# Optimization experiments

Measured on AMD Instinct MI355X. Metric: run time of the kernel, lower is better.

Reference implementation:

```python
import jax, jax.numpy as jnp
import numpy as np

EMBED_DIM = 64
GAMMA = 1.0
N_X = 8192
N_Y = 8192


def _self_attention(inputs, W_q, W_k):
    # inputs: [n, d]; W_q, W_k: [d, d]
    q = inputs @ W_q
    k = inputs @ W_k
    scores = jax.nn.softmax(q @ k.T / jnp.sqrt(jnp.float32(EMBED_DIM)), axis=-1)  # [n, n]
    return scores @ inputs  # [n, d]


def setup_inputs() -> dict:
    key = jax.random.key(0)
    k1, k2, k3, k4 = jax.random.split(key, 4)
    return {
        "rotation_params": jax.random.normal(k1, (EMBED_DIM, EMBED_DIM), dtype=jnp.float32),
        "entangle_params": jax.random.normal(k2, (EMBED_DIM, EMBED_DIM), dtype=jnp.float32),
        "x": jax.random.normal(k3, (N_X, EMBED_DIM), dtype=jnp.float32),
        "y": jax.random.normal(k4, (N_Y, EMBED_DIM), dtype=jnp.float32),
    }


def reference(rotation_params, entangle_params, x, y):
    x_att = _self_attention(x, rotation_params, entangle_params)  # [n_x, d]
    y_att = _self_attention(y, rotation_params, entangle_params)  # [n_y, d]
    # Pairwise squared distances, vectorizing the original per-pair loop.
    diff = x_att[:, None, :] - y_att[None, :, :]  # [n_x, n_y, d]
    sq = jnp.sum(diff * diff, axis=-1)  # [n_x, n_y]
    return jnp.exp(-GAMMA * sq)
```

## Files before the change

### kernel.cpp

```cpp
#include <hip/hip_runtime.h>
#include <math.h>

#define N 8192
#define D 64
#define LOG2E 1.4426950408889634f

typedef _Float16 half_t;
typedef _Float16 f16x8 __attribute__((ext_vector_type(8)));
typedef _Float16 f16x4 __attribute__((ext_vector_type(4)));
typedef float f32x4 __attribute__((ext_vector_type(4)));

#define MFMA32(a, b, c) __builtin_amdgcn_mfma_f32_16x16x32_f16((a), (b), (c), 0, 0, 0)

#define SPLIT(v, H, L) { half_t _h = (half_t)(v); (H) = _h; (L) = (half_t)((v) - (float)_h); }


__global__ __launch_bounds__(256) void proj_kernel(
    const float* __restrict__ Wq, const float* __restrict__ Wk,
    const float* __restrict__ X, const float* __restrict__ Y,
    float* __restrict__ Qx, float* __restrict__ Qy,
    half_t* __restrict__ Kfx, half_t* __restrict__ Kfy)
{
    __shared__ float sWq[64][64];
    __shared__ float sWk[64][64];
    __shared__ float sIn[16][64];
    const int t = threadIdx.x;
#pragma unroll
    for (int p = 0; p < 16; ++p) {
        int idx = p * 256 + t;
        sWq[idx >> 6][idx & 63] = Wq[idx];
        sWk[idx >> 6][idx & 63] = Wk[idx];
    }
    const int R0 = blockIdx.x * 16;
    const float* src; float* dq; half_t* dkf; int r0;
    if (R0 < N) { src = X; dq = Qx; dkf = Kfx; r0 = R0; }
    else        { src = Y; dq = Qy; dkf = Kfy; r0 = R0 - N; }
#pragma unroll
    for (int p = 0; p < 4; ++p) {
        int idx = p * 256 + t;
        sIn[idx >> 6][idx & 63] = src[(size_t)r0 * D + idx];
    }
    __syncthreads();
    const int c = t & 63;
    const int rb = t >> 6;
    const int ksi = c >> 5, quadi = (c >> 3) & 3, j = c & 7;
#pragma unroll
    for (int rr = 0; rr < 4; ++rr) {
        int r = rr * 4 + rb;
        float aq = 0.f, ak = 0.f;
#pragma unroll
        for (int k = 0; k < 64; ++k) {
            float xv = sIn[r][k];
            aq = fmaf(xv, sWq[k][c], aq);
            ak = fmaf(xv, sWk[k][c], ak);
        }
        int rg = r0 + r;
        dq[(size_t)rg * D + c] = aq * (0.125f * LOG2E);
        int tile = rg >> 5, tau = (rg >> 4) & 1, c16l = rg & 15;
        size_t kidx = (size_t)tile * 4096 + ksi * 2048 + tau * 1024
                    + (quadi * 16 + c16l) * 8 + j;
        half_t hh = (half_t)ak;
        dkf[kidx]       = hh;
        dkf[kidx + 512] = (half_t)(ak - (float)hh);
    }
}

__global__ __launch_bounds__(256) void ztprep_kernel(
    const float* __restrict__ X, const float* __restrict__ Y,
    half_t* __restrict__ Zfx, half_t* __restrict__ Zfy)
{
    const int t = threadIdx.x;
    const int tile = blockIdx.x;
    const float* src = blockIdx.y ? Y : X;
    half_t* dst = blockIdx.y ? Zfy : Zfx;
    const int dt = t >> 6, lane = t & 63;
    const int quad = lane >> 4, c16 = lane & 15;
    f16x8 h;
#pragma unroll
    for (int j = 0; j < 8; ++j)
        h[j] = (half_t)src[(size_t)(tile * 32 + quad * 8 + j) * D + dt * 16 + c16];
    *(f16x8*)&dst[(size_t)tile * 2048 + dt * 512 + lane * 8] = h;
}

template<int KS>
__global__ __launch_bounds__(256, 2) void attn_kernel(
    const float* __restrict__ Qx, const float* __restrict__ Qy,
    const half_t* __restrict__ Kfx, const half_t* __restrict__ Kfy,
    const half_t* __restrict__ Zfx, const half_t* __restrict__ Zfy,
    float* __restrict__ Opart, float* __restrict__ mpart, float* __restrict__ lpart)
{
    const int side = blockIdx.y;
    const float*  Q  = side ? Qy  : Qx;
    const half_t* Kf = side ? Kfy : Kfx;
    const half_t* Zf = side ? Zfy : Zfx;
    const int t = threadIdx.x, w = t >> 6, lane = t & 63;
    const int c16 = lane & 15, quad = lane >> 4;
    const int q0 = blockIdx.x * 128 + w * 32;
    const int tile0 = blockIdx.z * (N / KS / 32);
    const int ITERS = (N / KS) / 32;

    __shared__ half_t Pbuf[4][32][40];
    half_t (*Phi)[40] = Pbuf[w];

    f16x8 qh[2][2], ql[2][2];
#pragma unroll
    for (int qg = 0; qg < 2; ++qg)
#pragma unroll
        for (int ks = 0; ks < 2; ++ks) {
            const float* s = &Q[(size_t)(q0 + 16 * qg + c16) * D + ks * 32 + quad * 8];
            f32x4 v0 = *(const f32x4*)s;
            f32x4 v1 = *(const f32x4*)(s + 4);
            f16x8 h, l;
#pragma unroll
            for (int i = 0; i < 4; ++i) { SPLIT(v0[i], h[i],     l[i]); }
#pragma unroll
            for (int i = 0; i < 4; ++i) { SPLIT(v1[i], h[4 + i], l[4 + i]); }
            qh[qg][ks] = h; ql[qg][ks] = l;
        }

    f32x4 ot[4][2] = {};
    f32x4 lacc[2] = {};
    float m_run[2] = {-INFINITY, -INFINITY};
    f16x8 ones;
#pragma unroll
    for (int i = 0; i < 8; ++i) ones[i] = (half_t)1.0f;

    f16x8 kAh[2][2], kAl[2][2], kBh[2][2], kBl[2][2];
    f32x4 st[2][2];

    auto loadK = [&](int tile, f16x8 (&kh)[2][2], f16x8 (&kl)[2][2]) {
        const half_t* b = Kf + (size_t)tile * 4096 + lane * 8;
#pragma unroll
        for (int ks = 0; ks < 2; ++ks)
#pragma unroll
            for (int tau = 0; tau < 2; ++tau) {
                kh[ks][tau] = *(const f16x8*)&b[ks * 2048 + tau * 1024];
                kl[ks][tau] = *(const f16x8*)&b[ks * 2048 + tau * 1024 + 512];
            }
    };
    auto doS = [&](f16x8 (&kh)[2][2], f16x8 (&kl)[2][2]) {
        const f32x4 zero = {};
#pragma unroll
        for (int qg = 0; qg < 2; ++qg)
#pragma unroll
            for (int tau = 0; tau < 2; ++tau) st[qg][tau] = zero;
#pragma unroll
        for (int ks = 0; ks < 2; ++ks)
#pragma unroll
            for (int tau = 0; tau < 2; ++tau)
#pragma unroll
                for (int qg = 0; qg < 2; ++qg) {
                    st[qg][tau] = MFMA32(kh[ks][tau], qh[qg][ks], st[qg][tau]);
                    st[qg][tau] = MFMA32(kh[ks][tau], ql[qg][ks], st[qg][tau]);
                    st[qg][tau] = MFMA32(kl[ks][tau], qh[qg][ks], st[qg][tau]);
                }
    };

    auto body = [&](int tt, f16x8 (&kh2)[2][2], f16x8 (&kl2)[2][2]) {
        const int tile = tile0 + tt;
        const half_t* zb = Zf + (size_t)tile * 2048 + lane * 8;
        f16x8 zh[4];
#pragma unroll
        for (int dt = 0; dt < 4; ++dt)
            zh[dt] = *(const f16x8*)&zb[dt * 512];
        const bool more = (tt + 1 < ITERS);
        if (more) loadK(tile + 1, kh2, kl2);
#pragma unroll
        for (int qg = 0; qg < 2; ++qg) {
            float mt = fmaxf(fmaxf(fmaxf(st[qg][0][0], st[qg][0][1]),
                                   fmaxf(st[qg][0][2], st[qg][0][3])),
                             fmaxf(fmaxf(st[qg][1][0], st[qg][1][1]),
                                   fmaxf(st[qg][1][2], st[qg][1][3])));
            mt = fmaxf(mt, __shfl_xor(mt, 16));
            mt = fmaxf(mt, __shfl_xor(mt, 32));
            float mn = fmaxf(m_run[qg], mt);
            float al = exp2f(m_run[qg] - mn);
            m_run[qg] = mn;
#pragma unroll
            for (int tau = 0; tau < 2; ++tau) {
                f16x4 h4;
#pragma unroll
                for (int r = 0; r < 4; ++r)
                    h4[r] = (half_t)exp2f(st[qg][tau][r] - mn);
                *(f16x4*)&Phi[16 * qg + c16][16 * tau + 4 * quad] = h4;
            }
            lacc[qg] *= al;
#pragma unroll
            for (int dt = 0; dt < 4; ++dt) ot[dt][qg] *= al;
        }
        f16x8 pbh[2];
#pragma unroll
        for (int qg = 0; qg < 2; ++qg)
            pbh[qg] = *(const f16x8*)&Phi[16 * qg + c16][quad * 8];
#pragma unroll
        for (int dt = 0; dt < 4; ++dt)
#pragma unroll
            for (int qg = 0; qg < 2; ++qg)
                ot[dt][qg] = MFMA32(zh[dt], pbh[qg], ot[dt][qg]);
#pragma unroll
        for (int qg = 0; qg < 2; ++qg)
            lacc[qg] = MFMA32(ones, pbh[qg], lacc[qg]);
        if (more) doS(kh2, kl2);
    };

    loadK(tile0, kAh, kAl);
    doS(kAh, kAl);
#pragma unroll 1
    for (int tt = 0; tt < ITERS; tt += 2) {
        body(tt,     kBh, kBl);
        body(tt + 1, kAh, kAl);
    }

    const size_t obase = (size_t)(side * KS + blockIdx.z) * N;
#pragma unroll
    for (int qg = 0; qg < 2; ++qg) {
        int q = q0 + 16 * qg + c16;
#pragma unroll
        for (int dt = 0; dt < 4; ++dt)
            *(f32x4*)&Opart[(obase + q) * D + 16 * dt + 4 * quad] = ot[dt][qg];
        if (quad == 0) {
            mpart[obase + q] = m_run[qg];
            lpart[obase + q] = lacc[qg][0];
        }
    }
}

template<int KS>
__global__ __launch_bounds__(256) void combine_kernel(
    const float* __restrict__ Opart, const float* __restrict__ mpart,
    const float* __restrict__ lpart,
    half_t* __restrict__ Xf, half_t* __restrict__ Yf,
    float* __restrict__ n2x, float* __restrict__ n2y)
{
    const int side = blockIdx.y;
    const int q = blockIdx.x * 16 + (threadIdx.x >> 4);
    const int d4 = (threadIdx.x & 15) * 4;
    float m[KS], l[KS];
#pragma unroll
    for (int s = 0; s < KS; ++s) {
        size_t b = (size_t)(side * KS + s) * N + q;
        m[s] = mpart[b]; l[s] = lpart[b];
    }
    float M = -INFINITY;
#pragma unroll
    for (int s = 0; s < KS; ++s) M = fmaxf(M, m[s]);
    float L = 0.f;
    f32x4 o = {0.f, 0.f, 0.f, 0.f};
#pragma unroll
    for (int s = 0; s < KS; ++s) {
        float sc = exp2f(m[s] - M);
        L += l[s] * sc;
        f32x4 p = *(const f32x4*)&Opart[((size_t)(side * KS + s) * N + q) * D + d4];
        o += p * sc;
    }
    float inv = 1.f / L;
    o *= inv;
    float sq = o[0] * o[0] + o[1] * o[1] + o[2] * o[2] + o[3] * o[3];
#pragma unroll
    for (int off = 1; off < 16; off <<= 1) sq += __shfl_xor(sq, off);
    half_t* dst = side ? Yf : Xf;
    float*  n2  = side ? n2y : n2x;
    if ((threadIdx.x & 15) == 0) n2[q] = sq * LOG2E;
    const float oscale = side ? 1.0f : 2.0f * LOG2E;
    f16x4 h4, l4;
#pragma unroll
    for (int i = 0; i < 4; ++i) { float v = o[i] * oscale; SPLIT(v, h4[i], l4[i]); }
    const int tile16 = q >> 4, c16l = q & 15;
    const int ksi = d4 >> 5, quadi = (d4 >> 3) & 3, j0 = d4 & 7;
    size_t idx = (size_t)tile16 * 2048 + ksi * 1024 + (quadi * 16 + c16l) * 8 + j0;
    *(f16x4*)&dst[idx]       = h4;
    *(f16x4*)&dst[idx + 512] = l4;
}

__global__ __launch_bounds__(256, 3) void rbf_kernel(
    const half_t* __restrict__ Xf, const half_t* __restrict__ Yf,
    const float* __restrict__ n2x, const float* __restrict__ n2y,
    float* __restrict__ out)
{
    const int t = threadIdx.x, w = t >> 6, lane = t & 63;
    const int c16 = lane & 15, quad = lane >> 4;
    const int X0 = blockIdx.y * 128 + (w >> 1) * 64;
    const int Y0 = blockIdx.x * 128 + (w & 1) * 64;
    float ny[4];
    f32x4 nx4[4];
#pragma unroll
    for (int yt = 0; yt < 4; ++yt) ny[yt] = n2y[Y0 + 16 * yt + c16];
#pragma unroll
    for (int xt = 0; xt < 4; ++xt)
        nx4[xt] = *(const f32x4*)&n2x[X0 + 16 * xt + 4 * quad];

    const half_t* Xb = Xf + lane * 8;
    const half_t* Yb = Yf + lane * 8;
    f32x4 acc[4][4] = {};
#pragma unroll
    for (int ks = 0; ks < 2; ++ks) {
        f16x8 bh[4], bl[4];
#pragma unroll
        for (int yt = 0; yt < 4; ++yt) {
            size_t off = (size_t)((Y0 >> 4) + yt) * 2048 + ks * 1024;
            bh[yt] = *(const f16x8*)&Yb[off];
            bl[yt] = *(const f16x8*)&Yb[off + 512];
        }
#pragma unroll
        for (int xt = 0; xt < 4; ++xt) {
            size_t ao = (size_t)((X0 >> 4) + xt) * 2048 + ks * 1024;
            f16x8 ah = *(const f16x8*)&Xb[ao];
            f16x8 al = *(const f16x8*)&Xb[ao + 512];
#pragma unroll
            for (int yt = 0; yt < 4; ++yt) {
                acc[xt][yt] = MFMA32(ah, bh[yt], acc[xt][yt]);
                acc[xt][yt] = MFMA32(ah, bl[yt], acc[xt][yt]);
                acc[xt][yt] = MFMA32(al, bh[yt], acc[xt][yt]);
            }
        }
    }
#pragma unroll
    for (int xt = 0; xt < 4; ++xt)
#pragma unroll
        for (int r = 0; r < 4; ++r) {
            int xr = X0 + 16 * xt + 4 * quad + r;
            float nx = nx4[xt][r];
#pragma unroll
            for (int yt = 0; yt < 4; ++yt) {
                float v = exp2f(acc[xt][yt][r] - nx - ny[yt]);
                out[(size_t)xr * N + Y0 + 16 * yt + c16] = v;
            }
        }
}

extern "C" void kernel_launch(void* const* d_in, const int* in_sizes, int n_in,
                              void* d_out, int out_size, void* d_ws, size_t ws_size,
                              hipStream_t stream) {
    const float* Wq = (const float*)d_in[0];
    const float* Wk = (const float*)d_in[1];
    const float* x  = (const float*)d_in[2];
    const float* y  = (const float*)d_in[3];
    float* out = (float*)d_out;

    char* p = (char*)d_ws;
    size_t used = 0;
    auto alloc = [&](size_t bytes) -> void* {
        void* r = (void*)(p + used);
        used += (bytes + 255) & ~(size_t)255;
        return r;
    };
    float*  Qx  = (float*) alloc((size_t)N * D * 4);
    float*  Qy  = (float*) alloc((size_t)N * D * 4);
    half_t* Kfx = (half_t*)alloc((size_t)N * D * 2 * 2);
    half_t* Kfy = (half_t*)alloc((size_t)N * D * 2 * 2);
    half_t* Zfx = (half_t*)alloc((size_t)N * D * 2);
    half_t* Zfy = (half_t*)alloc((size_t)N * D * 2);
    half_t* Xf  = (half_t*)alloc((size_t)N * D * 2 * 2);
    half_t* Yf  = (half_t*)alloc((size_t)N * D * 2 * 2);
    float*  n2x = (float*) alloc((size_t)N * 4);
    float*  n2y = (float*) alloc((size_t)N * 4);

    const size_t base = used;
    const size_t per_split = (size_t)2 * N * D * 4 + (size_t)2 * N * 4 * 2 + 3 * 256;
    int KS = 4;
    if      (ws_size >= base + 16 * per_split) KS = 16;
    else if (ws_size >= base +  8 * per_split) KS = 8;

    float* Opart = (float*)alloc((size_t)2 * KS * N * D * 4);
    float* mpart = (float*)alloc((size_t)2 * KS * N * 4);
    float* lpart = (float*)alloc((size_t)2 * KS * N * 4);

    proj_kernel<<<dim3(2 * N / 16), 256, 0, stream>>>(Wq, Wk, x, y, Qx, Qy, Kfx, Kfy);
    ztprep_kernel<<<dim3(N / 32, 2), 256, 0, stream>>>(x, y, Zfx, Zfy);
    if (KS == 16) {
        attn_kernel<16><<<dim3(N / 128, 2, 16), 256, 0, stream>>>(
            Qx, Qy, Kfx, Kfy, Zfx, Zfy, Opart, mpart, lpart);
        combine_kernel<16><<<dim3(N / 16, 2), 256, 0, stream>>>(
            Opart, mpart, lpart, Xf, Yf, n2x, n2y);
    } else if (KS == 8) {
        attn_kernel<8><<<dim3(N / 128, 2, 8), 256, 0, stream>>>(
            Qx, Qy, Kfx, Kfy, Zfx, Zfy, Opart, mpart, lpart);
        combine_kernel<8><<<dim3(N / 16, 2), 256, 0, stream>>>(
            Opart, mpart, lpart, Xf, Yf, n2x, n2y);
    } else {
        attn_kernel<4><<<dim3(N / 128, 2, 4), 256, 0, stream>>>(
            Qx, Qy, Kfx, Kfy, Zfx, Zfy, Opart, mpart, lpart);
        combine_kernel<4><<<dim3(N / 16, 2), 256, 0, stream>>>(
            Opart, mpart, lpart, Xf, Yf, n2x, n2y);
    }
    rbf_kernel<<<dim3(N / 128, N / 128), 256, 0, stream>>>(Xf, Yf, n2x, n2y, out);
}
```

Baseline: 428.8 us.

## Pre-split Q in projection, software-pipeline attention scores, single-fp16 RBF GEMM

The projection kernel now writes Q as pre-split fp16 hi/lo in MFMA fragment layout, so the attention kernel loads it directly instead of converting fp32. The attention loop double-buffers the score tiles so the next tile's QK MFMAs are issued before the current softmax, and K is prefetched two tiles ahead. Separately, the combine kernel stores attention outputs as a single fp16 value (no lo part), with norms computed from the rounded values, so the RBF GEMM issues one MFMA per tile instead of three and reads half the data. The RBF kernel's occupancy hint rises to 4. Dropping the split trades accuracy in the distance computation for less compute, and the extra score buffer adds register pressure.

```diff
diff --git a/kernel.cpp b/kernel.cpp
--- a/kernel.cpp
+++ b/kernel.cpp
@@ -18,7 +18,7 @@
 __global__ __launch_bounds__(256) void proj_kernel(
     const float* __restrict__ Wq, const float* __restrict__ Wk,
     const float* __restrict__ X, const float* __restrict__ Y,
-    float* __restrict__ Qx, float* __restrict__ Qy,
+    half_t* __restrict__ Qfx, half_t* __restrict__ Qfy,
     half_t* __restrict__ Kfx, half_t* __restrict__ Kfy)
 {
     __shared__ float sWq[64][64];
@@ -32,9 +32,9 @@
         sWk[idx >> 6][idx & 63] = Wk[idx];
     }
     const int R0 = blockIdx.x * 16;
-    const float* src; float* dq; half_t* dkf; int r0;
-    if (R0 < N) { src = X; dq = Qx; dkf = Kfx; r0 = R0; }
-    else        { src = Y; dq = Qy; dkf = Kfy; r0 = R0 - N; }
+    const float* src; half_t* dqf; half_t* dkf; int r0;
+    if (R0 < N) { src = X; dqf = Qfx; dkf = Kfx; r0 = R0; }
+    else        { src = Y; dqf = Qfy; dkf = Kfy; r0 = R0 - N; }
 #pragma unroll
     for (int p = 0; p < 4; ++p) {
         int idx = p * 256 + t;
@@ -54,14 +54,17 @@
             aq = fmaf(xv, sWq[k][c], aq);
             ak = fmaf(xv, sWk[k][c], ak);
         }
+        aq *= (0.125f * LOG2E);
         int rg = r0 + r;
-        dq[(size_t)rg * D + c] = aq * (0.125f * LOG2E);
         int tile = rg >> 5, tau = (rg >> 4) & 1, c16l = rg & 15;
-        size_t kidx = (size_t)tile * 4096 + ksi * 2048 + tau * 1024
-                    + (quadi * 16 + c16l) * 8 + j;
-        half_t hh = (half_t)ak;
-        dkf[kidx]       = hh;
-        dkf[kidx + 512] = (half_t)(ak - (float)hh);
+        size_t idx = (size_t)tile * 4096 + ksi * 2048 + tau * 1024
+                   + (quadi * 16 + c16l) * 8 + j;
+        half_t qhh = (half_t)aq;
+        dqf[idx]       = qhh;
+        dqf[idx + 512] = (half_t)(aq - (float)qhh);
+        half_t khh = (half_t)ak;
+        dkf[idx]       = khh;
+        dkf[idx + 512] = (half_t)(ak - (float)khh);
     }
 }
 
@@ -84,13 +87,13 @@
 
 template<int KS>
 __global__ __launch_bounds__(256, 2) void attn_kernel(
-    const float* __restrict__ Qx, const float* __restrict__ Qy,
+    const half_t* __restrict__ Qfx, const half_t* __restrict__ Qfy,
     const half_t* __restrict__ Kfx, const half_t* __restrict__ Kfy,
     const half_t* __restrict__ Zfx, const half_t* __restrict__ Zfy,
     float* __restrict__ Opart, float* __restrict__ mpart, float* __restrict__ lpart)
 {
     const int side = blockIdx.y;
-    const float*  Q  = side ? Qy  : Qx;
+    const half_t* Qf = side ? Qfy : Qfx;
     const half_t* Kf = side ? Kfy : Kfx;
     const half_t* Zf = side ? Zfy : Zfx;
     const int t = threadIdx.x, w = t >> 6, lane = t & 63;
@@ -103,20 +106,16 @@
     half_t (*Phi)[40] = Pbuf[w];
 
     f16x8 qh[2][2], ql[2][2];
-#pragma unroll
-    for (int qg = 0; qg < 2; ++qg)
-#pragma unroll
-        for (int ks = 0; ks < 2; ++ks) {
-            const float* s = &Q[(size_t)(q0 + 16 * qg + c16) * D + ks * 32 + quad * 8];
-            f32x4 v0 = *(const f32x4*)s;
-            f32x4 v1 = *(const f32x4*)(s + 4);
-            f16x8 h, l;
-#pragma unroll
-            for (int i = 0; i < 4; ++i) { SPLIT(v0[i], h[i],     l[i]); }
-#pragma unroll
-            for (int i = 0; i < 4; ++i) { SPLIT(v1[i], h[4 + i], l[4 + i]); }
-            qh[qg][ks] = h; ql[qg][ks] = l;
-        }
+    {
+        const half_t* qb = Qf + (size_t)(q0 >> 5) * 4096 + lane * 8;
+#pragma unroll
+        for (int ks = 0; ks < 2; ++ks)
+#pragma unroll
+            for (int qg = 0; qg < 2; ++qg) {
+                qh[qg][ks] = *(const f16x8*)&qb[ks * 2048 + qg * 1024];
+                ql[qg][ks] = *(const f16x8*)&qb[ks * 2048 + qg * 1024 + 512];
+            }
+    }
 
     f32x4 ot[4][2] = {};
     f32x4 lacc[2] = {};
@@ -126,7 +125,7 @@
     for (int i = 0; i < 8; ++i) ones[i] = (half_t)1.0f;
 
     f16x8 kAh[2][2], kAl[2][2], kBh[2][2], kBl[2][2];
-    f32x4 st[2][2];
+    f32x4 stA[2][2], stB[2][2];
 
     auto loadK = [&](int tile, f16x8 (&kh)[2][2], f16x8 (&kl)[2][2]) {
         const half_t* b = Kf + (size_t)tile * 4096 + lane * 8;
@@ -138,7 +137,7 @@
                 kl[ks][tau] = *(const f16x8*)&b[ks * 2048 + tau * 1024 + 512];
             }
     };
-    auto doS = [&](f16x8 (&kh)[2][2], f16x8 (&kl)[2][2]) {
+    auto doS = [&](f32x4 (&st)[2][2], f16x8 (&kh)[2][2], f16x8 (&kl)[2][2]) {
         const f32x4 zero = {};
 #pragma unroll
         for (int qg = 0; qg < 2; ++qg)
@@ -156,21 +155,22 @@
                 }
     };
 
-    auto body = [&](int tt, f16x8 (&kh2)[2][2], f16x8 (&kl2)[2][2]) {
-        const int tile = tile0 + tt;
-        const half_t* zb = Zf + (size_t)tile * 2048 + lane * 8;
+    auto body = [&](int tt, f32x4 (&stCur)[2][2], f32x4 (&stNext)[2][2],
+                    f16x8 (&kNh)[2][2], f16x8 (&kNl)[2][2],
+                    f16x8 (&kRh)[2][2], f16x8 (&kRl)[2][2]) {
+        if (tt + 1 < ITERS) doS(stNext, kNh, kNl);
+        if (tt + 2 < ITERS) loadK(tile0 + tt + 2, kRh, kRl);
+        const half_t* zb = Zf + (size_t)(tile0 + tt) * 2048 + lane * 8;
         f16x8 zh[4];
 #pragma unroll
         for (int dt = 0; dt < 4; ++dt)
             zh[dt] = *(const f16x8*)&zb[dt * 512];
-        const bool more = (tt + 1 < ITERS);
-        if (more) loadK(tile + 1, kh2, kl2);
 #pragma unroll
         for (int qg = 0; qg < 2; ++qg) {
-            float mt = fmaxf(fmaxf(fmaxf(st[qg][0][0], st[qg][0][1]),
-                                   fmaxf(st[qg][0][2], st[qg][0][3])),
-                             fmaxf(fmaxf(st[qg][1][0], st[qg][1][1]),
-                                   fmaxf(st[qg][1][2], st[qg][1][3])));
+            float mt = fmaxf(fmaxf(fmaxf(stCur[qg][0][0], stCur[qg][0][1]),
+                                   fmaxf(stCur[qg][0][2], stCur[qg][0][3])),
+                             fmaxf(fmaxf(stCur[qg][1][0], stCur[qg][1][1]),
+                                   fmaxf(stCur[qg][1][2], stCur[qg][1][3])));
             mt = fmaxf(mt, __shfl_xor(mt, 16));
             mt = fmaxf(mt, __shfl_xor(mt, 32));
             float mn = fmaxf(m_run[qg], mt);
@@ -181,7 +181,7 @@
                 f16x4 h4;
 #pragma unroll
                 for (int r = 0; r < 4; ++r)
-                    h4[r] = (half_t)exp2f(st[qg][tau][r] - mn);
+                    h4[r] = (half_t)exp2f(stCur[qg][tau][r] - mn);
                 *(f16x4*)&Phi[16 * qg + c16][16 * tau + 4 * quad] = h4;
             }
             lacc[qg] *= al;
@@ -200,15 +200,15 @@
 #pragma unroll
         for (int qg = 0; qg < 2; ++qg)
             lacc[qg] = MFMA32(ones, pbh[qg], lacc[qg]);
-        if (more) doS(kh2, kl2);
     };
 
     loadK(tile0, kAh, kAl);
-    doS(kAh, kAl);
+    doS(stA, kAh, kAl);
+    if (ITERS > 1) loadK(tile0 + 1, kBh, kBl);
 #pragma unroll 1
     for (int tt = 0; tt < ITERS; tt += 2) {
-        body(tt,     kBh, kBl);
-        body(tt + 1, kAh, kAl);
+        body(tt,     stA, stB, kBh, kBl, kAh, kAl);
+        body(tt + 1, stB, stA, kAh, kAl, kBh, kBl);
     }
 
     const size_t obase = (size_t)(side * KS + blockIdx.z) * N;
@@ -253,26 +253,25 @@
         f32x4 p = *(const f32x4*)&Opart[((size_t)(side * KS + s) * N + q) * D + d4];
         o += p * sc;
     }
-    float inv = 1.f / L;
-    o *= inv;
-    float sq = o[0] * o[0] + o[1] * o[1] + o[2] * o[2] + o[3] * o[3];
+    const float oscale = (side ? 1.0f : 2.0f * LOG2E) / L;
+    f16x4 h4;
+#pragma unroll
+    for (int i = 0; i < 4; ++i) h4[i] = (half_t)(o[i] * oscale);
+    float sq = 0.f;
+#pragma unroll
+    for (int i = 0; i < 4; ++i) { float hv = (float)h4[i]; sq = fmaf(hv, hv, sq); }
 #pragma unroll
     for (int off = 1; off < 16; off <<= 1) sq += __shfl_xor(sq, off);
     half_t* dst = side ? Yf : Xf;
     float*  n2  = side ? n2y : n2x;
-    if ((threadIdx.x & 15) == 0) n2[q] = sq * LOG2E;
-    const float oscale = side ? 1.0f : 2.0f * LOG2E;
-    f16x4 h4, l4;
-#pragma unroll
-    for (int i = 0; i < 4; ++i) { float v = o[i] * oscale; SPLIT(v, h4[i], l4[i]); }
+    if ((threadIdx.x & 15) == 0)
+        n2[q] = side ? sq * LOG2E : sq * (0.25f / LOG2E);
     const int tile16 = q >> 4, c16l = q & 15;
     const int ksi = d4 >> 5, quadi = (d4 >> 3) & 3, j0 = d4 & 7;
-    size_t idx = (size_t)tile16 * 2048 + ksi * 1024 + (quadi * 16 + c16l) * 8 + j0;
-    *(f16x4*)&dst[idx]       = h4;
-    *(f16x4*)&dst[idx + 512] = l4;
-}
-
-__global__ __launch_bounds__(256, 3) void rbf_kernel(
+    *(f16x4*)&dst[(size_t)tile16 * 1024 + ksi * 512 + (quadi * 16 + c16l) * 8 + j0] = h4;
+}
+
+__global__ __launch_bounds__(256, 4) void rbf_kernel(
     const half_t* __restrict__ Xf, const half_t* __restrict__ Yf,
     const float* __restrict__ n2x, const float* __restrict__ n2y,
     float* __restrict__ out)
@@ -294,24 +293,16 @@
     f32x4 acc[4][4] = {};
 #pragma unroll
     for (int ks = 0; ks < 2; ++ks) {
-        f16x8 bh[4], bl[4];
-#pragma unroll
-        for (int yt = 0; yt < 4; ++yt) {
-            size_t off = (size_t)((Y0 >> 4) + yt) * 2048 + ks * 1024;
-            bh[yt] = *(const f16x8*)&Yb[off];
-            bl[yt] = *(const f16x8*)&Yb[off + 512];
-        }
+        f16x8 bh[4];
+#pragma unroll
+        for (int yt = 0; yt < 4; ++yt)
+            bh[yt] = *(const f16x8*)&Yb[(size_t)((Y0 >> 4) + yt) * 1024 + ks * 512];
 #pragma unroll
         for (int xt = 0; xt < 4; ++xt) {
-            size_t ao = (size_t)((X0 >> 4) + xt) * 2048 + ks * 1024;
-            f16x8 ah = *(const f16x8*)&Xb[ao];
-            f16x8 al = *(const f16x8*)&Xb[ao + 512];
-#pragma unroll
-            for (int yt = 0; yt < 4; ++yt) {
+            f16x8 ah = *(const f16x8*)&Xb[(size_t)((X0 >> 4) + xt) * 1024 + ks * 512];
+#pragma unroll
+            for (int yt = 0; yt < 4; ++yt)
                 acc[xt][yt] = MFMA32(ah, bh[yt], acc[xt][yt]);
-                acc[xt][yt] = MFMA32(ah, bl[yt], acc[xt][yt]);
-                acc[xt][yt] = MFMA32(al, bh[yt], acc[xt][yt]);
-            }
         }
     }
 #pragma unroll
@@ -344,14 +335,14 @@
         used += (bytes + 255) & ~(size_t)255;
         return r;
     };
-    float*  Qx  = (float*) alloc((size_t)N * D * 4);
-    float*  Qy  = (float*) alloc((size_t)N * D * 4);
+    half_t* Qfx = (half_t*)alloc((size_t)N * D * 2 * 2);
+    half_t* Qfy = (half_t*)alloc((size_t)N * D * 2 * 2);
     half_t* Kfx = (half_t*)alloc((size_t)N * D * 2 * 2);
     half_t* Kfy = (half_t*)alloc((size_t)N * D * 2 * 2);
     half_t* Zfx = (half_t*)alloc((size_t)N * D * 2);
     half_t* Zfy = (half_t*)alloc((size_t)N * D * 2);
-    half_t* Xf  = (half_t*)alloc((size_t)N * D * 2 * 2);
-    half_t* Yf  = (half_t*)alloc((size_t)N * D * 2 * 2);
+    half_t* Xf  = (half_t*)alloc((size_t)N * D * 2);
+    half_t* Yf  = (half_t*)alloc((size_t)N * D * 2);
     float*  n2x = (float*) alloc((size_t)N * 4);
     float*  n2y = (float*) alloc((size_t)N * 4);
 
@@ -365,21 +356,22 @@
     float* mpart = (float*)alloc((size_t)2 * KS * N * 4);
     float* lpart = (float*)alloc((size_t)2 * KS * N * 4);
 
-    proj_kernel<<<dim3(2 * N / 16), 256, 0, stream>>>(Wq, Wk, x, y, Qx, Qy, Kfx, Kfy);
+    proj_kernel<<<dim3(2 * N / 16), 256, 0, stream>>>(Wq, Wk, x, y,
+                                                      Qfx, Qfy, Kfx, Kfy);
     ztprep_kernel<<<dim3(N / 32, 2), 256, 0, stream>>>(x, y, Zfx, Zfy);
     if (KS == 16) {
         attn_kernel<16><<<dim3(N / 128, 2, 16), 256, 0, stream>>>(
-            Qx, Qy, Kfx, Kfy, Zfx, Zfy, Opart, mpart, lpart);
+            Qfx, Qfy, Kfx, Kfy, Zfx, Zfy, Opart, mpart, lpart);
         combine_kernel<16><<<dim3(N / 16, 2), 256, 0, stream>>>(
             Opart, mpart, lpart, Xf, Yf, n2x, n2y);
     } else if (KS == 8) {
         attn_kernel<8><<<dim3(N / 128, 2, 8), 256, 0, stream>>>(
-            Qx, Qy, Kfx, Kfy, Zfx, Zfy, Opart, mpart, lpart);
+            Qfx, Qfy, Kfx, Kfy, Zfx, Zfy, Opart, mpart, lpart);
         combine_kernel<8><<<dim3(N / 16, 2), 256, 0, stream>>>(
             Opart, mpart, lpart, Xf, Yf, n2x, n2y);
     } else {
         attn_kernel<4><<<dim3(N / 128, 2, 4), 256, 0, stream>>>(
-            Qx, Qy, Kfx, Kfy, Zfx, Zfy, Opart, mpart, lpart);
+            Qfx, Qfy, Kfx, Kfy, Zfx, Zfy, Opart, mpart, lpart);
         combine_kernel<4><<<dim3(N / 16, 2), 256, 0, stream>>>(
             Opart, mpart, lpart, Xf, Yf, n2x, n2y);
     }
```

New measurement: 392.6 us. -8.4%, faster.
